# Performance work log

Hardware: AMD Instinct MI355X
Metric: run time of the kernel (lower is better)

## Reference

```python
import jax, jax.numpy as jnp
import numpy as np

N = 200000          # real (non-pad) faces
P = 8192            # pad entries
PAD = N + P         # padded table size
C_IN = 128
C_OUT = 128


def setup_inputs() -> dict:
    key = jax.random.key(0)
    ks = jax.random.split(key, 6)
    x = jax.random.normal(ks[0], (N, C_IN), jnp.float32)
    # column 0 = the face itself (a real, non-pad index); columns 1..8 = neighbors
    col0 = jnp.arange(N, dtype=jnp.int64)[:, None]
    nbrs = jax.random.randint(ks[1], (N, 8), 0, PAD, dtype=jnp.int64)
    face_neighborhood = jnp.concatenate([col0, nbrs], axis=1)
    face_is_pad = jnp.arange(PAD) >= N  # last P rows are padding
    s = 1.0 / np.sqrt(C_IN).astype(np.float32)
    in_proj_w = jax.random.normal(ks[2], (3 * C_IN, C_IN), jnp.float32) * s
    in_proj_b = jnp.zeros((3 * C_IN,), jnp.float32)
    out_proj_w = jax.random.normal(ks[3], (C_IN, C_IN), jnp.float32) * s
    out_proj_b = jnp.zeros((C_IN,), jnp.float32)
    conv_w = jax.random.normal(ks[4], (C_OUT, C_IN, 1, 2), jnp.float32) * (1.0 / np.sqrt(2.0 * C_IN).astype(np.float32))
    conv_b = jnp.zeros((C_OUT,), jnp.float32)
    return {
        "x": x,
        "face_neighborhood": face_neighborhood,
        "face_is_pad": face_is_pad,
        "pad_size": PAD,
        "in_proj_w": in_proj_w,
        "in_proj_b": in_proj_b,
        "out_proj_w": out_proj_w,
        "out_proj_b": out_proj_b,
        "conv_w": conv_w,
        "conv_b": conv_b,
    }


def reference(x, face_neighborhood, face_is_pad, pad_size,
              in_proj_w, in_proj_b, out_proj_w, out_proj_b, conv_w, conv_b):
    C = x.shape[1]
    H = max(1, C // 32)
    Dh = C // H
    # scatter real features into the padded table (padded_x[~face_is_pad] = x)
    nonpad_idx = jnp.nonzero(~face_is_pad, size=x.shape[0])[0]
    padded_x = jnp.zeros((pad_size, C), x.dtype).at[nonpad_idx].set(x)
    f = padded_x[face_neighborhood]              # [N, 9, C] 9-way gather
    center = f[:, 0]                             # [N, C] query feature
    kv = f[:, 1:]                                # [N, 8, C]
    # torch MultiheadAttention: packed in_proj then per-head scaled dot-product
    q = (center @ in_proj_w[:C].T + in_proj_b[:C]).reshape(-1, 1, H, Dh).transpose(0, 2, 1, 3)       # [N,H,1,Dh]
    k = (kv @ in_proj_w[C:2 * C].T + in_proj_b[C:2 * C]).reshape(-1, 8, H, Dh).transpose(0, 2, 1, 3)  # [N,H,8,Dh]
    v = (kv @ in_proj_w[2 * C:].T + in_proj_b[2 * C:]).reshape(-1, 8, H, Dh).transpose(0, 2, 1, 3)    # [N,H,8,Dh]
    scale = 1.0 / jnp.sqrt(jnp.asarray(Dh, q.dtype))
    scores = jnp.einsum('nhqd,nhkd->nhqk', q, k) * scale  # [N,H,1,8]
    pad_mask = face_is_pad[face_neighborhood[:, 1:]][:, None, None, :]  # [N,1,1,8]
    scores = jnp.where(pad_mask, -jnp.inf, scores)
    attn = jax.nn.softmax(scores, axis=-1)
    o = jnp.einsum('nhqk,nhkd->nhqd', attn, v)            # [N,H,1,Dh]
    o = o.transpose(0, 2, 1, 3).reshape(-1, C)            # [N,C] (q_len==1)
    h = o @ out_proj_w.T + out_proj_b                     # [N,C]
    # Conv2d(C_in, C_out, (1,2)) over [N, C, 1, 2] == linear fuse of center & h
    out = center @ conv_w[:, :, 0, 0].T + h @ conv_w[:, :, 0, 1].T + conv_b  # [N, C_out]
    return out
```

## Files before the change

### kernel.cpp

```cpp
#include <hip/hip_runtime.h>

typedef __bf16 bfrag __attribute__((ext_vector_type(8)));
typedef float f32x4 __attribute__((ext_vector_type(4)));

__device__ __forceinline__ unsigned short f2bf(float f) {
  unsigned u = __float_as_uint(f);
  u = (u + 0x7fffu + ((u >> 16) & 1u)) >> 16;
  return (unsigned short)u;
}
__device__ __forceinline__ float bflo(unsigned u) { return __uint_as_float(u << 16); }
__device__ __forceinline__ float bfhi(unsigned u) { return __uint_as_float(u & 0xffff0000u); }

__global__ void k_prep(const float* __restrict__ in_proj_w,
                       const float* __restrict__ conv_w,
                       const float* __restrict__ out_proj_w,
                       const float* __restrict__ out_proj_b,
                       const float* __restrict__ conv_b,
                       unsigned short* __restrict__ WcatF,
                       unsigned short* __restrict__ W2F,
                       float* __restrict__ cvec) {
  int b = blockIdx.x, t = threadIdx.x;
  if (b < 384) {
    unsigned short v = f2bf(in_proj_w[b * 128 + t]);
    int cb = b >> 7, r7 = b & 127;
    int cB = r7 >> 4, mr = r7 & 15;
    int ks = t >> 5, quad = (t >> 3) & 3, j = t & 7;
    WcatF[(((cb * 8 + cB) * 4 + ks) << 9) + (quad * 16 + mr) * 8 + j] = v;
    return;
  }
  const int c = b - 384;
  const int cB = c >> 4, mr = c & 15;
  __shared__ float cw[128];
  __shared__ float red[2];
  cw[t] = conv_w[(c * 128 + t) * 2 + 1];
  __syncthreads();

  float a[8] = {0.f, 0.f, 0.f, 0.f, 0.f, 0.f, 0.f, 0.f};
#pragma unroll
  for (int kk = 0; kk < 16; ++kk)
#pragma unroll
    for (int u = 0; u < 8; ++u)
      a[u] += cw[kk * 8 + u] * out_proj_w[(kk * 8 + u) * 128 + t];
  float s = ((a[0] + a[1]) + (a[2] + a[3])) + ((a[4] + a[5]) + (a[6] + a[7]));

  {
    int kc = t >> 6, ks2 = (t >> 5) & 1, quad = (t >> 3) & 3, j = t & 7;
    W2F[(((cB * 4 + kc) * 2 + ks2) << 9) + (quad * 16 + mr) * 8 + j] = f2bf(s);
  }
  {
    int K = 128 + t;
    int kc = K >> 6, ks2 = (K >> 5) & 1, quad = (K >> 3) & 3, j = K & 7;
    W2F[(((cB * 4 + kc) * 2 + ks2) << 9) + (quad * 16 + mr) * 8 + j] =
        f2bf(conv_w[(c * 128 + t) * 2]);
  }

  float p = cw[t] * out_proj_b[t];
#pragma unroll
  for (int d = 1; d < 64; d <<= 1) p += __shfl_xor(p, d);
  if ((t & 63) == 0) red[t >> 6] = p;
  __syncthreads();
  if (t == 0) cvec[c] = conv_b[c] + red[0] + red[1];
}

__global__ __launch_bounds__(256, 4) void k_gemm_qkv(
    const float* __restrict__ x, const unsigned short* __restrict__ WcatF,
    const float* __restrict__ in_proj_b, unsigned short* __restrict__ Qb,
    unsigned short* __restrict__ KVb, int M) {
  __shared__ unsigned short se[4][32 * 72];
  const int m0 = blockIdx.x * 128;
  const int t = threadIdx.x;
  const int w = t >> 6, lane = t & 63, quad = lane >> 4, mr = lane & 15;
  unsigned short* sew = se[w];

  bfrag af[4][2];
#pragma unroll
  for (int ks = 0; ks < 4; ++ks)
#pragma unroll
    for (int r = 0; r < 2; ++r) {
      int row = m0 + w * 32 + r * 16 + mr;
      union { unsigned short s[8]; bfrag f; } u;
      if (row < M) {
        const float4* p =
            reinterpret_cast<const float4*>(&x[(size_t)row * 128 + ks * 32 + quad * 8]);
        float4 v0 = p[0], v1 = p[1];
        u.s[0] = f2bf(v0.x); u.s[1] = f2bf(v0.y); u.s[2] = f2bf(v0.z); u.s[3] = f2bf(v0.w);
        u.s[4] = f2bf(v1.x); u.s[5] = f2bf(v1.y); u.s[6] = f2bf(v1.z); u.s[7] = f2bf(v1.w);
      } else {
#pragma unroll
        for (int i = 0; i < 8; ++i) u.s[i] = 0;
      }
      af[ks][r] = u.f;
    }

#pragma unroll
  for (int cb = 0; cb < 3; ++cb) {
    unsigned short* dst = (cb == 0) ? Qb : KVb;
    const int ldst = (cb == 0) ? 128 : 256;
    const int cb_off = (cb == 2) ? 128 : 0;
#pragma unroll
    for (int half = 0; half < 2; ++half) {
      f32x4 acc[2][4];
#pragma unroll
      for (int r = 0; r < 2; ++r)
#pragma unroll
        for (int c = 0; c < 4; ++c) acc[r][c] = (f32x4){0.f, 0.f, 0.f, 0.f};
#pragma unroll
      for (int ks = 0; ks < 4; ++ks)
#pragma unroll
        for (int c = 0; c < 4; ++c) {
          union { uint4 v; bfrag f; } u;
          u.v = *reinterpret_cast<const uint4*>(
              &WcatF[(((cb * 8 + half * 4 + c) * 4 + ks) << 9) + lane * 8]);
          acc[0][c] = __builtin_amdgcn_mfma_f32_16x16x32_bf16(af[ks][0], u.f, acc[0][c], 0, 0, 0);
          acc[1][c] = __builtin_amdgcn_mfma_f32_16x16x32_bf16(af[ks][1], u.f, acc[1][c], 0, 0, 0);
        }
      const float* bias = in_proj_b + cb * 128 + half * 64;
#pragma unroll
      for (int r = 0; r < 2; ++r)
#pragma unroll
        for (int c = 0; c < 4; ++c) {
          float bv = bias[c * 16 + mr];
#pragma unroll
          for (int g = 0; g < 4; ++g)
            sew[(r * 16 + quad * 4 + g) * 72 + c * 16 + mr] = f2bf(acc[r][c][g] + bv);
        }
#pragma unroll
      for (int i = 0; i < 4; ++i) {
        int ch = i * 64 + lane;
        int row = ch >> 3, cp = ch & 7;
        int grow = m0 + w * 32 + row;
        if (grow < M) {
          uint4 v = *reinterpret_cast<const uint4*>(&sew[row * 72 + cp * 8]);
          *reinterpret_cast<uint4*>(
              &dst[(size_t)grow * ldst + cb_off + half * 64 + cp * 8]) = v;
        }
      }
    }
  }
}

__global__ __launch_bounds__(256) void k_attn(
    const unsigned short* __restrict__ Qb, const unsigned short* __restrict__ KVb,
    const int* __restrict__ fn, unsigned short* __restrict__ Ob, int M) {
  const int w = threadIdx.x >> 6, lane = threadIdx.x & 63;
  const int hf = lane >> 5, l5 = lane & 31;
  const int n = blockIdx.x * 8 + w * 2 + hf;
  if (n >= M) return;
  const float scale = 0.17677669529663687f;
  uint2 qp = *reinterpret_cast<const uint2*>(&Qb[(size_t)n * 128 + 4 * l5]);
  float q0 = bflo(qp.x), q1 = bfhi(qp.x), q2 = bflo(qp.y), q3 = bfhi(qp.y);
  int idx[8];
#pragma unroll
  for (int j = 0; j < 8; ++j) idx[j] = fn[n * 9 + 1 + j];
  float o0 = 0.f, o1 = 0.f, o2 = 0.f, o3 = 0.f, sum = 0.f;
#pragma unroll
  for (int j = 0; j < 8; ++j) {
    bool valid = idx[j] < M;
    int id = valid ? idx[j] : 0;
    const unsigned short* rowp = &KVb[(size_t)id * 256 + 4 * l5];
    uint2 kk = *reinterpret_cast<const uint2*>(rowp);
    uint2 vv = *reinterpret_cast<const uint2*>(rowp + 128);
    float k0 = bflo(kk.x), k1 = bfhi(kk.x), k2 = bflo(kk.y), k3 = bfhi(kk.y);
    float p = q0 * k0 + q1 * k1 + q2 * k2 + q3 * k3;
    p += __shfl_xor(p, 1);
    p += __shfl_xor(p, 2);
    p += __shfl_xor(p, 4);
    float s = valid ? p * scale : -1e30f;
    float e = __expf(s);
    sum += e;
    float v0 = bflo(vv.x), v1 = bfhi(vv.x), v2 = bflo(vv.y), v3 = bfhi(vv.y);
    o0 += e * v0; o1 += e * v1; o2 += e * v2; o3 += e * v3;
  }
  float inv = 1.f / sum;
  union { unsigned short s[4]; uint2 u; } pk;
  pk.s[0] = f2bf(o0 * inv); pk.s[1] = f2bf(o1 * inv);
  pk.s[2] = f2bf(o2 * inv); pk.s[3] = f2bf(o3 * inv);
  *reinterpret_cast<uint2*>(&Ob[(size_t)n * 128 + 4 * l5]) = pk.u;
}

__global__ __launch_bounds__(256, 4) void k_gemm_out(
    const unsigned short* __restrict__ Ob, const float* __restrict__ x,
    const unsigned short* __restrict__ W2F, const float* __restrict__ cvec,
    float* __restrict__ out, int M) {
  __shared__ float sf[4][32 * 36];
  const int m0 = blockIdx.x * 128;
  const int t = threadIdx.x;
  const int w = t >> 6, lane = t & 63, quad = lane >> 4, mr = lane & 15;
  float* sfw = sf[w];

  f32x4 acc[2][8];
#pragma unroll
  for (int r = 0; r < 2; ++r)
#pragma unroll
    for (int c = 0; c < 8; ++c) acc[r][c] = (f32x4){0.f, 0.f, 0.f, 0.f};

#pragma unroll
  for (int kc = 0; kc < 4; ++kc) {
    bfrag af[2][2];
#pragma unroll
    for (int ks2 = 0; ks2 < 2; ++ks2)
#pragma unroll
      for (int r = 0; r < 2; ++r) {
        int row = m0 + w * 32 + r * 16 + mr;
        if (kc < 2) {
          union { uint4 v; bfrag f; } u;
          u.v = make_uint4(0u, 0u, 0u, 0u);
          if (row < M)
            u.v = *reinterpret_cast<const uint4*>(
                &Ob[(size_t)row * 128 + kc * 64 + ks2 * 32 + quad * 8]);
          af[ks2][r] = u.f;
        } else {
          union { unsigned short s[8]; bfrag f; } u;
          if (row < M) {
            const float4* p = reinterpret_cast<const float4*>(
                &x[(size_t)row * 128 + (kc - 2) * 64 + ks2 * 32 + quad * 8]);
            float4 v0 = p[0], v1 = p[1];
            u.s[0] = f2bf(v0.x); u.s[1] = f2bf(v0.y); u.s[2] = f2bf(v0.z); u.s[3] = f2bf(v0.w);
            u.s[4] = f2bf(v1.x); u.s[5] = f2bf(v1.y); u.s[6] = f2bf(v1.z); u.s[7] = f2bf(v1.w);
          } else {
#pragma unroll
            for (int i = 0; i < 8; ++i) u.s[i] = 0;
          }
          af[ks2][r] = u.f;
        }
      }
#pragma unroll
    for (int ks2 = 0; ks2 < 2; ++ks2)
#pragma unroll
      for (int c = 0; c < 8; ++c) {
        union { uint4 v; bfrag f; } u;
        u.v = *reinterpret_cast<const uint4*>(
            &W2F[(((c * 4 + kc) * 2 + ks2) << 9) + lane * 8]);
        acc[0][c] = __builtin_amdgcn_mfma_f32_16x16x32_bf16(af[ks2][0], u.f, acc[0][c], 0, 0, 0);
        acc[1][c] = __builtin_amdgcn_mfma_f32_16x16x32_bf16(af[ks2][1], u.f, acc[1][c], 0, 0, 0);
      }
  }
#pragma unroll
  for (int p = 0; p < 4; ++p) {
#pragma unroll
    for (int cc = 0; cc < 2; ++cc) {
      int c = p * 2 + cc;
      float cv = cvec[c * 16 + mr];
#pragma unroll
      for (int r = 0; r < 2; ++r)
#pragma unroll
        for (int g = 0; g < 4; ++g)
          sfw[(r * 16 + quad * 4 + g) * 36 + cc * 16 + mr] = acc[r][c][g] + cv;
    }
#pragma unroll
    for (int i = 0; i < 4; ++i) {
      int ch = i * 64 + lane;
      int row = ch >> 3, c4 = ch & 7;
      int grow = m0 + w * 32 + row;
      if (grow < M) {
        float4 v = *reinterpret_cast<const float4*>(&sfw[row * 36 + c4 * 4]);
        *reinterpret_cast<float4*>(&out[(size_t)grow * 128 + p * 32 + c4 * 4]) = v;
      }
    }
  }
}

extern "C" void kernel_launch(void* const* d_in, const int* in_sizes, int n_in,
                              void* d_out, int out_size, void* d_ws, size_t ws_size,
                              hipStream_t stream) {
  const float* x          = (const float*)d_in[0];
  const int*   fn         = (const int*)d_in[1];
  const float* in_proj_w  = (const float*)d_in[4];
  const float* in_proj_b  = (const float*)d_in[5];
  const float* out_proj_w = (const float*)d_in[6];
  const float* out_proj_b = (const float*)d_in[7];
  const float* conv_w     = (const float*)d_in[8];
  const float* conv_b     = (const float*)d_in[9];
  const int M = in_sizes[0] / 128;

  unsigned short* KVb = (unsigned short*)d_out;
  char* ws = (char*)d_ws;
  unsigned short* Qb    = (unsigned short*)ws;
  unsigned short* Ob    = (unsigned short*)(ws + (size_t)M * 128 * 2);
  unsigned short* WcatF = (unsigned short*)(ws + (size_t)M * 128 * 4);
  unsigned short* W2F   = WcatF + 384 * 128;
  float*          cvec  = (float*)(W2F + 128 * 256);

  const int mt = (M + 127) / 128;
  k_prep<<<dim3(512), dim3(128), 0, stream>>>(in_proj_w, conv_w, out_proj_w,
                                              out_proj_b, conv_b, WcatF, W2F, cvec);
  k_gemm_qkv<<<dim3(mt), dim3(256), 0, stream>>>(x, WcatF, in_proj_b, Qb, KVb, M);
  k_attn<<<dim3((M + 7) / 8), dim3(256), 0, stream>>>(Qb, KVb, fn, Ob, M);
  k_gemm_out<<<dim3(mt), dim3(256), 0, stream>>>(Ob, x, W2F, cvec, (float*)d_out, M);
}
```

Measured before the change: 433.7 us.

## Fuse attention with output projection GEMM into one kernel

Adds k_attn_out, which computes attention for 32 rows per block, stages the bf16 attention output in shared memory, and immediately runs the out-proj/conv MFMA GEMM against it and x. This removes the Ob round trip through global memory and one kernel launch. Because KV can no longer alias d_out, it now lives in the workspace when that is large enough, with the old path kept as a fallback. The fused block covers only 32 rows, so each block reloads W2F more often, and the attention phase may hide latency less well.

```diff
diff --git a/kernel.cpp b/kernel.cpp
--- a/kernel.cpp
+++ b/kernel.cpp
@@ -135,6 +135,129 @@
               &dst[(size_t)grow * ldst + cb_off + half * 64 + cp * 8]) = v;
         }
       }
+    }
+  }
+}
+
+__global__ __launch_bounds__(256) void k_attn_out(
+    const unsigned short* __restrict__ Qb, const unsigned short* __restrict__ KVb,
+    const int* __restrict__ fn, const float* __restrict__ x,
+    const unsigned short* __restrict__ W2F, const float* __restrict__ cvec,
+    float* __restrict__ out, int M) {
+  __shared__ char smem[18432];
+  unsigned short* Ow = reinterpret_cast<unsigned short*>(smem);
+  const int base = blockIdx.x * 32;
+  const int t = threadIdx.x;
+  const int w = t >> 6, lane = t & 63, quad = lane >> 4, mr = lane & 15;
+  const int hf = lane >> 5, l5 = lane & 31;
+  const float scale = 0.17677669529663687f;
+
+  for (int it = 0; it < 4; ++it) {
+    const int ri = it * 8 + w * 2 + hf;
+    const int n = base + ri;
+    union { unsigned short s[4]; uint2 u; } pk;
+    pk.u = make_uint2(0u, 0u);
+    if (n < M) {
+      unsigned long long q8 = __builtin_nontemporal_load(
+          reinterpret_cast<const unsigned long long*>(&Qb[(size_t)n * 128 + 4 * l5]));
+      float q0 = bflo((unsigned)q8), q1 = bfhi((unsigned)q8);
+      float q2 = bflo((unsigned)(q8 >> 32)), q3 = bfhi((unsigned)(q8 >> 32));
+      int idx[8];
+#pragma unroll
+      for (int j = 0; j < 8; ++j)
+        idx[j] = __builtin_nontemporal_load(&fn[n * 9 + 1 + j]);
+      float o0 = 0.f, o1 = 0.f, o2 = 0.f, o3 = 0.f, sum = 0.f;
+#pragma unroll
+      for (int j = 0; j < 8; ++j) {
+        bool valid = idx[j] < M;
+        int id = valid ? idx[j] : 0;
+        const unsigned short* rowp = &KVb[(size_t)id * 256 + 4 * l5];
+        uint2 kk = *reinterpret_cast<const uint2*>(rowp);
+        uint2 vv = *reinterpret_cast<const uint2*>(rowp + 128);
+        float k0 = bflo(kk.x), k1 = bfhi(kk.x), k2 = bflo(kk.y), k3 = bfhi(kk.y);
+        float p = q0 * k0 + q1 * k1 + q2 * k2 + q3 * k3;
+        p += __shfl_xor(p, 1);
+        p += __shfl_xor(p, 2);
+        p += __shfl_xor(p, 4);
+        float s = valid ? p * scale : -1e30f;
+        float e = __expf(s);
+        sum += e;
+        float v0 = bflo(vv.x), v1 = bfhi(vv.x), v2 = bflo(vv.y), v3 = bfhi(vv.y);
+        o0 += e * v0; o1 += e * v1; o2 += e * v2; o3 += e * v3;
+      }
+      float inv = 1.f / sum;
+      pk.s[0] = f2bf(o0 * inv); pk.s[1] = f2bf(o1 * inv);
+      pk.s[2] = f2bf(o2 * inv); pk.s[3] = f2bf(o3 * inv);
+    }
+    *reinterpret_cast<uint2*>(&Ow[ri * 136 + 4 * l5]) = pk.u;
+  }
+  __syncthreads();
+
+  f32x4 acc[2][2];
+#pragma unroll
+  for (int r = 0; r < 2; ++r)
+#pragma unroll
+    for (int c = 0; c < 2; ++c) acc[r][c] = (f32x4){0.f, 0.f, 0.f, 0.f};
+
+#pragma unroll
+  for (int kc = 0; kc < 4; ++kc) {
+    bfrag af[2][2];
+#pragma unroll
+    for (int ks2 = 0; ks2 < 2; ++ks2)
+#pragma unroll
+      for (int r = 0; r < 2; ++r) {
+        if (kc < 2) {
+          union { uint4 v; bfrag f; } u;
+          u.v = *reinterpret_cast<const uint4*>(
+              &Ow[(r * 16 + mr) * 136 + kc * 64 + ks2 * 32 + quad * 8]);
+          af[ks2][r] = u.f;
+        } else {
+          int row = base + r * 16 + mr;
+          union { unsigned short s[8]; bfrag f; } u;
+          if (row < M) {
+            const float4* p = reinterpret_cast<const float4*>(
+                &x[(size_t)row * 128 + (kc - 2) * 64 + ks2 * 32 + quad * 8]);
+            float4 v0 = p[0], v1 = p[1];
+            u.s[0] = f2bf(v0.x); u.s[1] = f2bf(v0.y); u.s[2] = f2bf(v0.z); u.s[3] = f2bf(v0.w);
+            u.s[4] = f2bf(v1.x); u.s[5] = f2bf(v1.y); u.s[6] = f2bf(v1.z); u.s[7] = f2bf(v1.w);
+          } else {
+#pragma unroll
+            for (int i = 0; i < 8; ++i) u.s[i] = 0;
+          }
+          af[ks2][r] = u.f;
+        }
+      }
+#pragma unroll
+    for (int ks2 = 0; ks2 < 2; ++ks2)
+#pragma unroll
+      for (int c2 = 0; c2 < 2; ++c2) {
+        union { uint4 v; bfrag f; } u;
+        u.v = *reinterpret_cast<const uint4*>(
+            &W2F[((((w * 2 + c2) * 4 + kc) * 2 + ks2) << 9) + lane * 8]);
+        acc[0][c2] = __builtin_amdgcn_mfma_f32_16x16x32_bf16(af[ks2][0], u.f, acc[0][c2], 0, 0, 0);
+        acc[1][c2] = __builtin_amdgcn_mfma_f32_16x16x32_bf16(af[ks2][1], u.f, acc[1][c2], 0, 0, 0);
+      }
+  }
+
+  __syncthreads();
+  float* sfw = reinterpret_cast<float*>(smem) + w * (32 * 36);
+#pragma unroll
+  for (int c2 = 0; c2 < 2; ++c2) {
+    float cv = cvec[(w * 2 + c2) * 16 + mr];
+#pragma unroll
+    for (int r = 0; r < 2; ++r)
+#pragma unroll
+      for (int g = 0; g < 4; ++g)
+        sfw[(r * 16 + quad * 4 + g) * 36 + c2 * 16 + mr] = acc[r][c2][g] + cv;
+  }
+#pragma unroll
+  for (int i = 0; i < 4; ++i) {
+    int ch = i * 64 + lane;
+    int row = ch >> 3, c4 = ch & 7;
+    int grow = base + row;
+    if (grow < M) {
+      float4 v = *reinterpret_cast<const float4*>(&sfw[row * 36 + c4 * 4]);
+      *reinterpret_cast<float4*>(&out[(size_t)grow * 128 + w * 32 + c4 * 4]) = v;
     }
   }
 }
@@ -272,19 +395,37 @@
   const float* conv_w     = (const float*)d_in[8];
   const float* conv_b     = (const float*)d_in[9];
   const int M = in_sizes[0] / 128;
-
-  unsigned short* KVb = (unsigned short*)d_out;
+  const int mt = (M + 127) / 128;
   char* ws = (char*)d_ws;
-  unsigned short* Qb    = (unsigned short*)ws;
-  unsigned short* Ob    = (unsigned short*)(ws + (size_t)M * 128 * 2);
-  unsigned short* WcatF = (unsigned short*)(ws + (size_t)M * 128 * 4);
-  unsigned short* W2F   = WcatF + 384 * 128;
-  float*          cvec  = (float*)(W2F + 128 * 256);
-
-  const int mt = (M + 127) / 128;
-  k_prep<<<dim3(512), dim3(128), 0, stream>>>(in_proj_w, conv_w, out_proj_w,
-                                              out_proj_b, conv_b, WcatF, W2F, cvec);
-  k_gemm_qkv<<<dim3(mt), dim3(256), 0, stream>>>(x, WcatF, in_proj_b, Qb, KVb, M);
-  k_attn<<<dim3((M + 7) / 8), dim3(256), 0, stream>>>(Qb, KVb, fn, Ob, M);
-  k_gemm_out<<<dim3(mt), dim3(256), 0, stream>>>(Ob, x, W2F, cvec, (float*)d_out, M);
-}
+
+  const size_t qbytes  = (size_t)M * 128 * 2;
+  const size_t kvbytes = (size_t)M * 256 * 2;
+  const size_t wbytes  = (size_t)(384 * 128 + 128 * 256) * 2 + 512;
+
+  if (ws_size >= qbytes + kvbytes + wbytes) {
+    unsigned short* Qb    = (unsigned short*)ws;
+    unsigned short* KVb   = (unsigned short*)(ws + qbytes);
+    unsigned short* WcatF = (unsigned short*)(ws + qbytes + kvbytes);
+    unsigned short* W2F   = WcatF + 384 * 128;
+    float*          cvec  = (float*)(W2F + 128 * 256);
+
+    k_prep<<<dim3(512), dim3(128), 0, stream>>>(in_proj_w, conv_w, out_proj_w,
+                                                out_proj_b, conv_b, WcatF, W2F, cvec);
+    k_gemm_qkv<<<dim3(mt), dim3(256), 0, stream>>>(x, WcatF, in_proj_b, Qb, KVb, M);
+    k_attn_out<<<dim3((M + 31) / 32), dim3(256), 0, stream>>>(
+        Qb, KVb, fn, x, W2F, cvec, (float*)d_out, M);
+  } else {
+    unsigned short* KVb   = (unsigned short*)d_out;
+    unsigned short* Qb    = (unsigned short*)ws;
+    unsigned short* Ob    = (unsigned short*)(ws + (size_t)M * 128 * 2);
+    unsigned short* WcatF = (unsigned short*)(ws + (size_t)M * 128 * 4);
+    unsigned short* W2F   = WcatF + 384 * 128;
+    float*          cvec  = (float*)(W2F + 128 * 256);
+
+    k_prep<<<dim3(512), dim3(128), 0, stream>>>(in_proj_w, conv_w, out_proj_w,
+                                                out_proj_b, conv_b, WcatF, W2F, cvec);
+    k_gemm_qkv<<<dim3(mt), dim3(256), 0, stream>>>(x, WcatF, in_proj_b, Qb, KVb, M);
+    k_attn<<<dim3((M + 7) / 8), dim3(256), 0, stream>>>(Qb, KVb, fn, Ob, M);
+    k_gemm_out<<<dim3(mt), dim3(256), 0, stream>>>(Ob, x, W2F, cvec, (float*)d_out, M);
+  }
+}
```

Measured after the change: 402.1 us. 7.3% less time.
